# Kernel tuning notes

Hardware: AMD Instinct MI355X
Metric: run time of the kernel (lower is better)

The kernel has to match this reference:

```python
import jax, jax.numpy as jnp
import numpy as np

B, S, HID = 4, 1024, 1024
NH = 16
DH = HID // NH  # 64


def _split_heads(t):
    # [B, S, HID] -> [B, NH, S, DH]
    return t.reshape(B, S, NH, DH).transpose(0, 2, 1, 3)


def _merge_heads(t):
    # [B, NH, S, DH] -> [B, S, HID]
    return t.transpose(0, 2, 1, 3).reshape(B, S, HID)


def setup_inputs() -> dict:
    key = jax.random.key(0)
    ks = jax.random.split(key, 13)
    scale = 1.0 / np.sqrt(HID)
    inp = {"x": jax.random.normal(ks[0], (B, S, HID), dtype=jnp.float32)}
    names = ["Wq", "Wk", "Wv", "Wq2", "Wk2", "Wv2"]
    for i, n in enumerate(names):
        inp[n] = jax.random.normal(ks[1 + i], (HID, HID), dtype=jnp.float32) * scale
        inp["b" + n[1:]] = jax.random.normal(ks[7 + i], (HID,), dtype=jnp.float32) * 0.01
    return inp


def _attn(q, k, v):
    # q,k,v: [B, NH, S, DH]
    scores = jnp.einsum("bhqd,bhkd->bhqk", q, k) / np.sqrt(DH).astype(np.float32)
    probs = jax.nn.softmax(scores, axis=-1)
    return jnp.einsum("bhqk,bhkd->bhqd", probs, v)


def reference(x, Wq, bq, Wk, bk, Wv, bv, Wq2, bq2, Wk2, bk2, Wv2, bv2):
    # nn.Linear: y = x @ W.T + b
    q1 = _split_heads(x @ Wq.T + bq)
    k1 = _split_heads(x @ Wk.T + bk)
    v1 = _split_heads(x @ Wv.T + bv)
    q2 = _split_heads(x @ Wq2.T + bq2)
    k2 = _split_heads(x @ Wk2.T + bk2)
    v2 = _split_heads(x @ Wv2.T + bv2)
    # 5'UTR direction: q1 attends to k2/v2; 3'UTR direction: q2 attends to k1/v1
    out5 = _merge_heads(_attn(q1, k2, v2))
    out3 = _merge_heads(_attn(q2, k1, v1))
    return (out5, out3)
```

## Files before the change

kernel.cpp:

```cpp
#include <hip/hip_runtime.h>


typedef __attribute__((ext_vector_type(8))) short bf16x8;
typedef __attribute__((ext_vector_type(4))) short bf16x4;
typedef __attribute__((ext_vector_type(4))) float f32x4;
typedef __attribute__((ext_vector_type(4))) short s16x4;

#define MFMA16(a, b, c) __builtin_amdgcn_mfma_f32_16x16x32_bf16(a, b, c, 0, 0, 0)
#define BARRIER() asm volatile("s_barrier" ::: "memory")
#define VMCNT0() asm volatile("s_waitcnt vmcnt(0)" ::: "memory")

__device__ __forceinline__ f32x4 mfma16k(bf16x4 a, bf16x4 b, f32x4 c) {
#if __has_builtin(__builtin_amdgcn_mfma_f32_16x16x16bf16_1k)
  return __builtin_amdgcn_mfma_f32_16x16x16bf16_1k(a, b, c, 0, 0, 0);
#elif __has_builtin(__builtin_amdgcn_mfma_f32_16x16x16_bf16)
  return __builtin_amdgcn_mfma_f32_16x16x16_bf16(a, b, c, 0, 0, 0);
#else
  asm volatile("v_mfma_f32_16x16x16_bf16 %0, %1, %2, %0"
               : "+v"(c) : "v"(a), "v"(b));
  return c;
#endif
}

__device__ __forceinline__ unsigned short f2bf(float f) {
  unsigned u = __float_as_uint(f);
  u = (u + 0x7fffu + ((u >> 16) & 1u)) >> 16;
  return (unsigned short)u;
}

__device__ __forceinline__ unsigned cvt_pk_bf16(float lo, float hi) {
  unsigned r;
  asm("v_cvt_pk_bf16_f32 %0, %1, %2" : "=v"(r) : "v"(lo), "v"(hi));
  return r;
}

__device__ __forceinline__ void gll16(const void* g, void* l) {
  __builtin_amdgcn_global_load_lds(
      (const __attribute__((address_space(1))) unsigned int*)g,
      (__attribute__((address_space(3))) unsigned int*)l, 16, 0, 0);
}

__global__ __launch_bounds__(256) void convert_k(
    const float* __restrict__ x,
    const float* __restrict__ W0, const float* __restrict__ W1,
    const float* __restrict__ W2, const float* __restrict__ W3,
    const float* __restrict__ W4, const float* __restrict__ W5,
    short* __restrict__ xbf, short* __restrict__ wbf) {
  const int tid = blockIdx.x * 256 + threadIdx.x;
  const int e = tid << 2;
  const float* src;
  short* dst;
  int off;
  if (e < (4 << 20)) {
    src = x; dst = xbf; off = e;
  } else {
    const int j = e - (4 << 20);
    const int wsel = j >> 20;
    off = j & ((1 << 20) - 1);
    src = (wsel == 0) ? W0 : (wsel == 1) ? W1 : (wsel == 2) ? W2
        : (wsel == 3) ? W3 : (wsel == 4) ? W4 : W5;
    dst = wbf + ((size_t)wsel << 20);
  }
  const float4 v = *(const float4*)(src + off);
  s16x4 o;
  o.x = (short)f2bf(v.x);
  o.y = (short)f2bf(v.y);
  o.z = (short)f2bf(v.z);
  o.w = (short)f2bf(v.w);
  *(s16x4*)(dst + off) = o;
}

__global__ __launch_bounds__(512, 2) void proj_gemm192(
    const short* __restrict__ Ag, const short* __restrict__ Wall,
    const float* __restrict__ bq, const float* __restrict__ bk,
    const float* __restrict__ bv, const float* __restrict__ bq2,
    const float* __restrict__ bk2, const float* __restrict__ bv2,
    short* __restrict__ qkv) {
  __shared__ __align__(16) short As[2][16384];
  __shared__ __align__(16) short Bs[2][12288];

  const int bid = blockIdx.x;
  const int xcd = bid & 7, k = bid >> 3;
  const int ns = k & 3, mb = k >> 2;
  const int nbase = (xcd * 4 + ns) * 192;
  const int m0 = mb << 8;

  const int t = threadIdx.x, lane = t & 63, w = t >> 6;
  const int g = lane >> 4, lr = lane & 15;
  const int wr = w >> 2, wc = w & 3;

  f32x4 acc[2][4][3] = {};

  auto stage_ah = [&](int T, int H) {
#pragma unroll
    for (int ld = 0; ld < 2; ++ld) {
      const int slot = (H << 10) + (ld << 9) + t;
      const int rr = slot >> 3;
      const int gc = (slot & 7) ^ (rr & 7);
      gll16(Ag + (size_t)(m0 + rr) * 1024 + (T << 6) + (gc << 3),
            &As[T & 1][slot * 8]);
    }
  };
  auto stage_b = [&](int T) {
#pragma unroll
    for (int ld = 0; ld < 3; ++ld) {
      const int slot = (ld << 9) + t;
      const int rr = slot >> 3;
      const int gc = (slot & 7) ^ (rr & 7);
      gll16(Wall + (size_t)(nbase + rr) * 1024 + (T << 6) + (gc << 3),
            &Bs[T & 1][slot * 8]);
    }
  };

  stage_ah(0, 0); stage_ah(0, 1); stage_b(0);
  VMCNT0();
  BARRIER();

#define LOAD_A(AV, MH, KK, TB)                                            \
  _Pragma("unroll") for (int mi = 0; mi < 4; ++mi) {                      \
    const int rA = wr * 128 + (MH) * 64 + mi * 16 + lr;                   \
    AV[mi] = *(const bf16x8*)                                             \
        &As[TB][rA * 64 + ((((KK) * 4 + g) ^ (rA & 7)) << 3)];            \
  }
#define LOAD_B(KK, TB)                                                    \
  _Pragma("unroll") for (int nj = 0; nj < 3; ++nj) {                      \
    const int rB = wc * 48 + nj * 16 + lr;                                \
    bf[nj] = *(const bf16x8*)                                             \
        &Bs[TB][rB * 64 + ((((KK) * 4 + g) ^ (rB & 7)) << 3)];            \
  }
#define MFMA_MH(MH, AV)                                                   \
  _Pragma("unroll") for (int mi = 0; mi < 4; ++mi)                        \
    _Pragma("unroll") for (int nj = 0; nj < 3; ++nj)                      \
      acc[MH][mi][nj] = MFMA16(AV[mi], bf[nj], acc[MH][mi][nj]);

  auto group = [&](int C, int TD, bool DV) {
    bf16x8 af0[4], af1[4], bf[3];
    {
      LOAD_A(af0, 0, 0, C); LOAD_A(af1, 1, 0, C); LOAD_B(0, C);
      if (DV) { stage_ah(TD, 0); stage_ah(TD, 1); }
      BARRIER();
      __builtin_amdgcn_s_setprio(1);
      MFMA_MH(0, af0);
      MFMA_MH(1, af1);
      __builtin_amdgcn_s_setprio(0);
      BARRIER();
    }
    {
      LOAD_A(af0, 0, 1, C); LOAD_A(af1, 1, 1, C); LOAD_B(1, C);
      if (DV) stage_b(TD);
      BARRIER();
      __builtin_amdgcn_s_setprio(1);
      MFMA_MH(0, af0);
      MFMA_MH(1, af1);
      __builtin_amdgcn_s_setprio(0);
      VMCNT0();
      BARRIER();
    }
  };

  for (int j = 0; j < 8; ++j) {
    group(0, 2 * j + 1, true);
    group(1, 2 * j + 2, j < 7);
  }

#undef LOAD_A
#undef LOAD_B
#undef MFMA_MH

#pragma unroll
  for (int nj = 0; nj < 3; ++nj) {
    const int nn = nbase + wc * 48 + nj * 16 + lr;
    const int p = nn >> 10, nl = nn & 1023;
    const float* bp = (p == 0) ? bq : (p == 1) ? bk : (p == 2) ? bv
                    : (p == 3) ? bq2 : (p == 4) ? bk2 : bv2;
    const float bb = bp[nl];
    const int h = nl >> 6, d = nl & 63;
    const int pt = (p == 0 || p == 3) ? 0 : (p == 1 || p == 4) ? 1 : 2;
    unsigned short* dst = (unsigned short*)qkv + ((size_t)p << 22);
#pragma unroll
    for (int mh = 0; mh < 2; ++mh) {
#pragma unroll
      for (int mi = 0; mi < 4; ++mi) {
#pragma unroll
        for (int r = 0; r < 4; ++r) {
          const int m = m0 + wr * 128 + mh * 64 + mi * 16 + (g << 2) + r;
          const int b = m >> 10, s = m & 1023;
          const unsigned short val = f2bf(acc[mh][mi][nj][r] + bb);
          size_t idx;
          if (pt == 0) {
            idx = ((size_t)(((b << 4) + h) * 1024 + s) << 6) + d;
          } else if (pt == 1) {
            const int d2 = (d & 7) | (((d >> 3) ^ (s & 7)) << 3);
            idx = ((size_t)(((b << 4) + h) * 1024 + s) << 6) + d2;
          } else {
            const int tt = s >> 6, s2 = s & 63;
            const int s3 = (s2 & 7) | (((s2 >> 3) ^ (d & 7)) << 3);
            idx = ((size_t)((((b << 4) + h) * 16 + tt) * 64 + d) << 6) + s3;
          }
          dst[idx] = val;
        }
      }
    }
  }
}

__global__ __launch_bounds__(512) void attn_k(const short* __restrict__ qkv,
                                              float* __restrict__ out) {
  __shared__ __align__(16) short Ks[2][64 * 64];
  __shared__ __align__(16) short Vs[2][64 * 64];

  const int L = blockIdx.x;
  const int xcd = L & 7, ss = L >> 3;
  const int qt = ss & 7, pg = ss >> 3;
  const int pp = xcd + (pg << 3);
  const int hb = pp & 63, dir = pp >> 6;

  const short* Q = qkv + ((size_t)(dir ? 3 : 0) << 22) + ((size_t)hb << 16);
  const short* K = qkv + ((size_t)(dir ? 1 : 4) << 22) + ((size_t)hb << 16);
  const short* V = qkv + ((size_t)(dir ? 2 : 5) << 22) + ((size_t)hb << 16);
  float* O = out + ((size_t)dir << 22);

  const int t = threadIdx.x, lane = t & 63, w = t >> 6;
  const int g = lane >> 4, lr = lane & 15;

  const int qrow = (qt << 7) + (w << 4) + lr;
  bf16x8 qf[2];
  qf[0] = *(const bf16x8*)(Q + qrow * 64 + g * 8);
  qf[1] = *(const bf16x8*)(Q + qrow * 64 + 32 + g * 8);

  const bf16x4 ones4 = {0x3F80, 0x3F80, 0x3F80, 0x3F80};

  f32x4 oacc[4] = {};
  f32x4 lacc = {};
  float mrun = -3.0e38f;
  const float CSC = 0.18033688f;

  const int srow = t >> 3;
  const int scol = (t & 7) << 3;

  auto stage = [&](int kt, int buf) {
    gll16(K + (size_t)((kt << 6) + srow) * 64 + scol, &Ks[buf][w << 9]);
    gll16(V + (size_t)(kt << 12) + (size_t)srow * 64 + scol, &Vs[buf][w << 9]);
  };

  stage(0, 0);
  VMCNT0();
  BARRIER();

  int cur = 0;
  for (int kt = 0; kt < 16; ++kt) {
    if (kt < 15) stage(kt + 1, cur ^ 1);

    f32x4 sc2[4] = {};
    __builtin_amdgcn_s_setprio(1);
#pragma unroll
    for (int dk = 0; dk < 2; ++dk) {
#pragma unroll
      for (int kn = 0; kn < 4; ++kn) {
        const int krow = kn * 16 + lr;
        const bf16x8 kf = *(const bf16x8*)
            &Ks[cur][krow * 64 +
                     ((((dk << 6) + (g << 4)) ^ ((krow & 7) << 4)) >> 1)];
        sc2[kn] = MFMA16(kf, qf[dk], sc2[kn]);
      }
    }
    __builtin_amdgcn_s_setprio(0);

    float tm = fmaxf(fmaxf(fmaxf(sc2[0][0], sc2[0][1]),
                           fmaxf(sc2[0][2], sc2[0][3])),
                     fmaxf(fmaxf(sc2[1][0], sc2[1][1]),
                           fmaxf(sc2[1][2], sc2[1][3])));
    tm = fmaxf(tm, fmaxf(fmaxf(fmaxf(sc2[2][0], sc2[2][1]),
                               fmaxf(sc2[2][2], sc2[2][3])),
                         fmaxf(fmaxf(sc2[3][0], sc2[3][1]),
                               fmaxf(sc2[3][2], sc2[3][3]))));
    const bool ok = __all(fmaf(tm, CSC, -mrun) <= 8.0f);
    if (!ok) {
      float t2 = fmaxf(tm, __shfl_xor(tm, 16));
      t2 = fmaxf(t2, __shfl_xor(t2, 32));
      const float mnew = fmaxf(mrun, t2 * CSC);
      const float scq = exp2f(mrun - mnew);
      mrun = mnew;
#pragma unroll
      for (int r = 0; r < 4; ++r) {
        const float sr = __shfl(scq, (g << 2) + r);
        lacc[r] *= sr;
#pragma unroll
        for (int dn = 0; dn < 4; ++dn) oacc[dn][r] *= sr;
      }
    }

    bf16x4 pa[4];
#pragma unroll
    for (int kn = 0; kn < 4; ++kn) {
      const float p0 = exp2f(fmaf(sc2[kn][0], CSC, -mrun));
      const float p1 = exp2f(fmaf(sc2[kn][1], CSC, -mrun));
      const float p2 = exp2f(fmaf(sc2[kn][2], CSC, -mrun));
      const float p3 = exp2f(fmaf(sc2[kn][3], CSC, -mrun));
      union { unsigned u[2]; bf16x4 v; } pk;
      pk.u[0] = cvt_pk_bf16(p0, p1);
      pk.u[1] = cvt_pk_bf16(p2, p3);
      pa[kn] = pk.v;
    }

    __builtin_amdgcn_s_setprio(1);
#pragma unroll
    for (int kn = 0; kn < 4; ++kn) {
      lacc = mfma16k(pa[kn], ones4, lacc);
#pragma unroll
      for (int dn = 0; dn < 4; ++dn) {
        const int vrow = dn * 16 + lr;
        const int ch = (2 * kn + (g >> 1)) ^ (vrow & 7);
        const bf16x4 vf = *(const bf16x4*)
            &Vs[cur][vrow * 64 + ch * 8 + ((g & 1) << 2)];
        oacc[dn] = mfma16k(pa[kn], vf, oacc[dn]);
      }
    }
    __builtin_amdgcn_s_setprio(0);

    VMCNT0();
    BARRIER();
    cur ^= 1;
  }

  const int b = hb >> 4, h = hb & 15;
  float rl[4];
#pragma unroll
  for (int r = 0; r < 4; ++r) rl[r] = 1.0f / lacc[r];
#pragma unroll
  for (int dn = 0; dn < 4; ++dn) {
#pragma unroll
    for (int r = 0; r < 4; ++r) {
      const int q = (qt << 7) + (w << 4) + (g << 2) + r;
      const int d = dn * 16 + lr;
      O[((size_t)(b * 1024 + q) << 10) + h * 64 + d] = oacc[dn][r] * rl[r];
    }
  }
}

extern "C" void kernel_launch(void* const* d_in, const int* in_sizes, int n_in,
                              void* d_out, int out_size, void* d_ws,
                              size_t ws_size, hipStream_t stream) {
  const float* x   = (const float*)d_in[0];
  const float* Wq  = (const float*)d_in[1];
  const float* bq  = (const float*)d_in[2];
  const float* Wk  = (const float*)d_in[3];
  const float* bk  = (const float*)d_in[4];
  const float* Wv  = (const float*)d_in[5];
  const float* bv  = (const float*)d_in[6];
  const float* Wq2 = (const float*)d_in[7];
  const float* bq2 = (const float*)d_in[8];
  const float* Wk2 = (const float*)d_in[9];
  const float* bk2 = (const float*)d_in[10];
  const float* Wv2 = (const float*)d_in[11];
  const float* bv2 = (const float*)d_in[12];

  char* ws = (char*)d_ws;
  short* xbf = (short*)ws;
  short* wbf = (short*)(ws + 8388608);
  short* qkv = (short*)(ws + 20971520);

  convert_k<<<10240, 256, 0, stream>>>(x, Wq, Wk, Wv, Wq2, Wk2, Wv2, xbf, wbf);
  proj_gemm192<<<512, 512, 0, stream>>>(xbf, wbf, bq, bk, bv, bq2, bk2,
                                        bv2, qkv);
  attn_k<<<1024, 512, 0, stream>>>(qkv, (float*)d_out);
}
```

Baseline: 155.2 us.

## Replace 256x192 projection GEMM with 128x192 tiles, BK=32 and 4 waves

```diff
diff --git a/kernel.cpp b/kernel.cpp
--- a/kernel.cpp
+++ b/kernel.cpp
@@ -70,106 +70,85 @@
   *(s16x4*)(dst + off) = o;
 }
 
-__global__ __launch_bounds__(512, 2) void proj_gemm192(
+__global__ __launch_bounds__(256, 3) void proj_hi(
     const short* __restrict__ Ag, const short* __restrict__ Wall,
     const float* __restrict__ bq, const float* __restrict__ bk,
     const float* __restrict__ bv, const float* __restrict__ bq2,
     const float* __restrict__ bk2, const float* __restrict__ bv2,
     short* __restrict__ qkv) {
-  __shared__ __align__(16) short As[2][16384];
-  __shared__ __align__(16) short Bs[2][12288];
+  __shared__ __align__(16) short As[2][128 * 32];
+  __shared__ __align__(16) short Bs[2][192 * 32];
 
   const int bid = blockIdx.x;
-  const int xcd = bid & 7, k = bid >> 3;
-  const int ns = k & 3, mb = k >> 2;
-  const int nbase = (xcd * 4 + ns) * 192;
-  const int m0 = mb << 8;
+  const int xcd = bid & 7, i = bid >> 3;
+  const int nbase = (xcd * 4 + (i >> 5)) * 192;
+  const int m0 = (i & 31) << 7;
 
   const int t = threadIdx.x, lane = t & 63, w = t >> 6;
   const int g = lane >> 4, lr = lane & 15;
-  const int wr = w >> 2, wc = w & 3;
-
-  f32x4 acc[2][4][3] = {};
-
-  auto stage_ah = [&](int T, int H) {
+
+  f32x4 acc[8][3] = {};
+
+#define SWZ(c, r) (((c) ^ ((r) & 3) ^ (((r) >> 2) & 3)) & 3)
+
+  auto stage = [&](int T, int buf) {
+    const int k0 = T << 5;
 #pragma unroll
     for (int ld = 0; ld < 2; ++ld) {
-      const int slot = (H << 10) + (ld << 9) + t;
-      const int rr = slot >> 3;
-      const int gc = (slot & 7) ^ (rr & 7);
-      gll16(Ag + (size_t)(m0 + rr) * 1024 + (T << 6) + (gc << 3),
-            &As[T & 1][slot * 8]);
+      const int slot = (ld << 8) + t;
+      const int rr = slot >> 2;
+      const int gc = SWZ(slot & 3, rr);
+      gll16(Ag + (size_t)(m0 + rr) * 1024 + k0 + (gc << 3),
+            &As[buf][slot * 8]);
+    }
+#pragma unroll
+    for (int ld = 0; ld < 3; ++ld) {
+      const int slot = (ld << 8) + t;
+      const int rr = slot >> 2;
+      const int gc = SWZ(slot & 3, rr);
+      gll16(Wall + (size_t)(nbase + rr) * 1024 + k0 + (gc << 3),
+            &Bs[buf][slot * 8]);
     }
   };
-  auto stage_b = [&](int T) {
-#pragma unroll
-    for (int ld = 0; ld < 3; ++ld) {
-      const int slot = (ld << 9) + t;
-      const int rr = slot >> 3;
-      const int gc = (slot & 7) ^ (rr & 7);
-      gll16(Wall + (size_t)(nbase + rr) * 1024 + (T << 6) + (gc << 3),
-            &Bs[T & 1][slot * 8]);
-    }
-  };
-
-  stage_ah(0, 0); stage_ah(0, 1); stage_b(0);
+
+  stage(0, 0);
   VMCNT0();
   BARRIER();
 
-#define LOAD_A(AV, MH, KK, TB)                                            \
-  _Pragma("unroll") for (int mi = 0; mi < 4; ++mi) {                      \
-    const int rA = wr * 128 + (MH) * 64 + mi * 16 + lr;                   \
-    AV[mi] = *(const bf16x8*)                                             \
-        &As[TB][rA * 64 + ((((KK) * 4 + g) ^ (rA & 7)) << 3)];            \
-  }
-#define LOAD_B(KK, TB)                                                    \
-  _Pragma("unroll") for (int nj = 0; nj < 3; ++nj) {                      \
-    const int rB = wc * 48 + nj * 16 + lr;                                \
-    bf[nj] = *(const bf16x8*)                                             \
-        &Bs[TB][rB * 64 + ((((KK) * 4 + g) ^ (rB & 7)) << 3)];            \
-  }
-#define MFMA_MH(MH, AV)                                                   \
-  _Pragma("unroll") for (int mi = 0; mi < 4; ++mi)                        \
-    _Pragma("unroll") for (int nj = 0; nj < 3; ++nj)                      \
-      acc[MH][mi][nj] = MFMA16(AV[mi], bf[nj], acc[MH][mi][nj]);
-
-  auto group = [&](int C, int TD, bool DV) {
-    bf16x8 af0[4], af1[4], bf[3];
-    {
-      LOAD_A(af0, 0, 0, C); LOAD_A(af1, 1, 0, C); LOAD_B(0, C);
-      if (DV) { stage_ah(TD, 0); stage_ah(TD, 1); }
-      BARRIER();
-      __builtin_amdgcn_s_setprio(1);
-      MFMA_MH(0, af0);
-      MFMA_MH(1, af1);
-      __builtin_amdgcn_s_setprio(0);
-      BARRIER();
-    }
-    {
-      LOAD_A(af0, 0, 1, C); LOAD_A(af1, 1, 1, C); LOAD_B(1, C);
-      if (DV) stage_b(TD);
-      BARRIER();
-      __builtin_amdgcn_s_setprio(1);
-      MFMA_MH(0, af0);
-      MFMA_MH(1, af1);
-      __builtin_amdgcn_s_setprio(0);
-      VMCNT0();
-      BARRIER();
-    }
-  };
-
-  for (int j = 0; j < 8; ++j) {
-    group(0, 2 * j + 1, true);
-    group(1, 2 * j + 2, j < 7);
-  }
-
-#undef LOAD_A
-#undef LOAD_B
-#undef MFMA_MH
+  int buf = 0;
+  for (int T = 0; T < 32; ++T) {
+    if (T < 31) stage(T + 1, buf ^ 1);
+
+    bf16x8 af[8], bf[3];
+#pragma unroll
+    for (int mi = 0; mi < 8; ++mi) {
+      const int rA = mi * 16 + lr;
+      af[mi] = *(const bf16x8*)&As[buf][rA * 32 + (SWZ(g, rA) << 3)];
+    }
+#pragma unroll
+    for (int nj = 0; nj < 3; ++nj) {
+      const int rB = w * 48 + nj * 16 + lr;
+      bf[nj] = *(const bf16x8*)&Bs[buf][rB * 32 + (SWZ(g, rB) << 3)];
+    }
+
+    __builtin_amdgcn_s_setprio(1);
+#pragma unroll
+    for (int mi = 0; mi < 8; ++mi)
+#pragma unroll
+      for (int nj = 0; nj < 3; ++nj)
+        acc[mi][nj] = MFMA16(af[mi], bf[nj], acc[mi][nj]);
+    __builtin_amdgcn_s_setprio(0);
+
+    VMCNT0();
+    BARRIER();
+    buf ^= 1;
+  }
+
+#undef SWZ
 
 #pragma unroll
   for (int nj = 0; nj < 3; ++nj) {
-    const int nn = nbase + wc * 48 + nj * 16 + lr;
+    const int nn = nbase + w * 48 + nj * 16 + lr;
     const int p = nn >> 10, nl = nn & 1023;
     const float* bp = (p == 0) ? bq : (p == 1) ? bk : (p == 2) ? bv
                     : (p == 3) ? bq2 : (p == 4) ? bk2 : bv2;
@@ -178,27 +157,24 @@
     const int pt = (p == 0 || p == 3) ? 0 : (p == 1 || p == 4) ? 1 : 2;
     unsigned short* dst = (unsigned short*)qkv + ((size_t)p << 22);
 #pragma unroll
-    for (int mh = 0; mh < 2; ++mh) {
-#pragma unroll
-      for (int mi = 0; mi < 4; ++mi) {
-#pragma unroll
-        for (int r = 0; r < 4; ++r) {
-          const int m = m0 + wr * 128 + mh * 64 + mi * 16 + (g << 2) + r;
-          const int b = m >> 10, s = m & 1023;
-          const unsigned short val = f2bf(acc[mh][mi][nj][r] + bb);
-          size_t idx;
-          if (pt == 0) {
-            idx = ((size_t)(((b << 4) + h) * 1024 + s) << 6) + d;
-          } else if (pt == 1) {
-            const int d2 = (d & 7) | (((d >> 3) ^ (s & 7)) << 3);
-            idx = ((size_t)(((b << 4) + h) * 1024 + s) << 6) + d2;
-          } else {
-            const int tt = s >> 6, s2 = s & 63;
-            const int s3 = (s2 & 7) | (((s2 >> 3) ^ (d & 7)) << 3);
-            idx = ((size_t)((((b << 4) + h) * 16 + tt) * 64 + d) << 6) + s3;
-          }
-          dst[idx] = val;
+    for (int mi = 0; mi < 8; ++mi) {
+#pragma unroll
+      for (int r = 0; r < 4; ++r) {
+        const int m = m0 + mi * 16 + (g << 2) + r;
+        const int b = m >> 10, s = m & 1023;
+        const unsigned short val = f2bf(acc[mi][nj][r] + bb);
+        size_t idx;
+        if (pt == 0) {
+          idx = ((size_t)(((b << 4) + h) * 1024 + s) << 6) + d;
+        } else if (pt == 1) {
+          const int d2 = (d & 7) | (((d >> 3) ^ (s & 7)) << 3);
+          idx = ((size_t)(((b << 4) + h) * 1024 + s) << 6) + d2;
+        } else {
+          const int tt = s >> 6, s2 = s & 63;
+          const int s3 = (s2 & 7) | (((s2 >> 3) ^ (d & 7)) << 3);
+          idx = ((size_t)((((b << 4) + h) * 16 + tt) * 64 + d) << 6) + s3;
         }
+        dst[idx] = val;
       }
     }
   }
@@ -361,7 +337,7 @@
   short* qkv = (short*)(ws + 20971520);
 
   convert_k<<<10240, 256, 0, stream>>>(x, Wq, Wk, Wv, Wq2, Wk2, Wv2, xbf, wbf);
-  proj_gemm192<<<512, 512, 0, stream>>>(xbf, wbf, bq, bk, bv, bq2, bk2,
-                                        bv2, qkv);
+  proj_hi<<<1024, 256, 0, stream>>>(xbf, wbf, bq, bk, bv, bq2, bk2,
+                                    bv2, qkv);
   attn_k<<<1024, 512, 0, stream>>>(qkv, (float*)d_out);
 }
```

Result: slower. 169.2 us (+9.0%).
